# Kernel tuning notes

Measured on AMD Instinct MI355X. Metric: run time of the kernel, lower is better.

The kernel has to match this reference:

```python
import jax, jax.numpy as jnp
import numpy as np

B, T, I, H, O = 128, 1024, 256, 512, 256


def setup_inputs() -> dict:
    key = jax.random.key(0)
    ks = jax.random.split(key, 6)
    fan_gate = I + H  # kaiming-style scaling for stability over long scan
    return {
        "input_seq": jax.random.normal(ks[0], (B, T, I), dtype=jnp.float32),
        "W_f": jax.random.normal(ks[1], (H, fan_gate), dtype=jnp.float32) / np.sqrt(fan_gate),
        "b_f": jnp.zeros((H,), dtype=jnp.float32),
        "W_i": jax.random.normal(ks[2], (H, fan_gate), dtype=jnp.float32) / np.sqrt(fan_gate),
        "b_i": jnp.zeros((H,), dtype=jnp.float32),
        "W_C": jax.random.normal(ks[3], (H, fan_gate), dtype=jnp.float32) / np.sqrt(fan_gate),
        "b_C": jnp.zeros((H,), dtype=jnp.float32),
        "W_o": jax.random.normal(ks[4], (H, fan_gate), dtype=jnp.float32) / np.sqrt(fan_gate),
        "b_o": jnp.zeros((H,), dtype=jnp.float32),
        "W_lin": jax.random.normal(ks[5], (O, H), dtype=jnp.float32) / np.sqrt(H),
        "b_lin": jnp.zeros((O,), dtype=jnp.float32),
    }


def reference(input_seq, W_f, b_f, W_i, b_i, W_C, b_C, W_o, b_o, W_lin, b_lin):
    batch = input_seq.shape[0]
    hidden = W_f.shape[0]

    def step(carry, x_t):
        h, C = carry  # [B,H] each
        combined = jnp.concatenate([x_t, h], axis=1)  # [B, I+H]
        f_t = jax.nn.sigmoid(combined @ W_f.T + b_f)
        i_t = jax.nn.sigmoid(combined @ W_i.T + b_i)
        C_tilde = jnp.tanh(combined @ W_C.T + b_C)
        o_t = jax.nn.sigmoid(combined @ W_o.T + b_o)
        C_new = f_t * C + i_t * C_tilde
        h_new = o_t * jnp.tanh(C_new)
        return (h_new, C_new), None

    h0 = jnp.zeros((batch, hidden), dtype=input_seq.dtype)
    C0 = jnp.zeros((batch, hidden), dtype=input_seq.dtype)
    # scan over time: input_seq -> [T, B, I]
    (h_T, _), _ = jax.lax.scan(step, (h0, C0), jnp.swapaxes(input_seq, 0, 1))
    return h_T @ W_lin.T + b_lin  # [B, O]
```

## Files before the change

kernel.cpp:

```cpp
#include <hip/hip_runtime.h>

#define BB 128
#define TT 1024
#define II 256
#define HH 512
#define OO 256
#define KK 768

typedef _Float16 half8 __attribute__((ext_vector_type(8)));
typedef _Float16 half4v __attribute__((ext_vector_type(4)));
typedef float f32x4 __attribute__((ext_vector_type(4)));
typedef unsigned u32x4 __attribute__((ext_vector_type(4)));
typedef unsigned long long u64_t;

__device__ __forceinline__ float sigm(float x) { return 1.f / (1.f + __expf(-x)); }
__device__ __forceinline__ float tanhfast(float x) {
  float e = __expf(-2.f * fabsf(x));
  return copysignf((1.f - e) / (1.f + e), x);
}

__global__ void __launch_bounds__(64)
prep_w(const float* __restrict__ Wf, const float* __restrict__ Wi,
       const float* __restrict__ Wc, const float* __restrict__ Wo,
       _Float16* __restrict__ W16)
{
  const int bid = blockIdx.x;
  const int ks = bid % 24, tile = bid / 24;
  const int lane = threadIdx.x;
  const int r = lane & 15, q = lane >> 4;
  const int lu = r >> 2, g = r & 3;
  const int unit = tile * 4 + lu;
  const float* Wg = (g == 0) ? Wf : (g == 1) ? Wi : (g == 2) ? Wc : Wo;
  const float* src = Wg + (size_t)unit * KK + ks * 32 + q * 8;
  float4 w0 = *(const float4*)src;
  float4 w1 = *(const float4*)(src + 4);
  half8 h;
  h[0] = (_Float16)w0.x; h[1] = (_Float16)w0.y; h[2] = (_Float16)w0.z; h[3] = (_Float16)w0.w;
  h[4] = (_Float16)w1.x; h[5] = (_Float16)w1.y; h[6] = (_Float16)w1.z; h[7] = (_Float16)w1.w;
  *(half8*)(W16 + ((size_t)bid * 64 + lane) * 8) = h;
}

__global__ void __launch_bounds__(256)
prep_x(const float* __restrict__ x, _Float16* __restrict__ x16)
{
  const int t = blockIdx.x;
  for (int i = threadIdx.x; i < BB * II / 4; i += 256) {
    const int b = i >> 6, c4 = (i & 63) * 4;
    float4 v = *(const float4*)(x + ((size_t)b * TT + t) * II + c4);
    half4v h;
    h[0] = (_Float16)v.x; h[1] = (_Float16)v.y; h[2] = (_Float16)v.z; h[3] = (_Float16)v.w;
    *(half4v*)(x16 + ((size_t)t * BB + b) * II + c4) = h;
  }
}

__device__ __forceinline__ unsigned pack2(unsigned a, unsigned b) {
  return (a & 0xffffu) | (b << 16);
}
__device__ __forceinline__ unsigned badtag(u32x4 g, unsigned ex) {
  return ((g.x ^ ex) | (g.y ^ ex) | (g.z ^ ex) | (g.w ^ ex)) & 0xFFFF0000u;
}

__global__ void __launch_bounds__(256, 1)
lstm_persist(const _Float16* __restrict__ x16, const _Float16* __restrict__ W16,
             const float* __restrict__ bfp, const float* __restrict__ bip,
             const float* __restrict__ bcp, const float* __restrict__ bop,
             const float* __restrict__ Wlin, const float* __restrict__ blin,
             float* __restrict__ out,
             unsigned* __restrict__ hbuf)
{
  __shared__ __align__(16) char hsb[2][16 * 1024];

  const int gid = blockIdx.x;
  const int p = gid & 7;
  const int ugh = gid >> 3;
  const int tid = threadIdx.x;
  const int wn = tid >> 6, lane = tid & 63;
  const int r = lane & 15, q = lane >> 4;
  const int lu = r >> 2, g4 = r & 3;
  const int rsw = (r & 7) << 4;

  half8 wfrag[24];
  {
    const half8* wp = (const half8*)W16 + (size_t)(ugh * 4 + wn) * 24 * 64 + lane;
#pragma unroll
    for (int ks = 0; ks < 24; ++ks) wfrag[ks] = wp[ks * 64];
  }

  const int unit = ugh * 16 + wn * 4 + lu;
  const float bfv = bfp[unit], biv = bip[unit], bcv = bcp[unit], bov = bop[unit];
  float C = 0.0f;
  const int arow = p * 16 + r;

  int unit0[4];
#pragma unroll
  for (int j = 0; j < 4; ++j) unit0[j] = 8 * (lane ^ ((4 * j + wn) & 7));

  f32x4 accN = {0.f, 0.f, 0.f, 0.f};
  {
    const _Float16* xr = x16 + (size_t)arow * II + q * 8;
#pragma unroll
    for (int ks = 0; ks < 8; ++ks) {
      half8 a = *(const half8*)(xr + ks * 32);
      accN = __builtin_amdgcn_mfma_f32_16x16x32_f16(a, wfrag[ks], accN, 0, 0, 0);
    }
  }

  for (int t = 0; t < TT; ++t) {
    f32x4 acc = accN;
    const int buf = t & 1;

    if (t > 0) {
      const unsigned ex32 = (unsigned)t << 16;
      const unsigned* b0 = hbuf + ((size_t)(buf * BB + p * 16) + 0 + wn) * HH + unit0[0];
      const unsigned* b1 = hbuf + ((size_t)(buf * BB + p * 16) + 4 + wn) * HH + unit0[1];
      const unsigned* b2 = hbuf + ((size_t)(buf * BB + p * 16) + 8 + wn) * HH + unit0[2];
      const unsigned* b3 = hbuf + ((size_t)(buf * BB + p * 16) + 12 + wn) * HH + unit0[3];
      u32x4 G0, G1, G2, G3, G4, G5, G6, G7;
      for (int it = 0;; ++it) {
        if ((it & 1) == 0) {
          asm volatile(
            "global_load_dwordx4 %0, %8, off sc0\n\t"
            "global_load_dwordx4 %1, %8, off offset:16 sc0\n\t"
            "global_load_dwordx4 %2, %9, off sc0\n\t"
            "global_load_dwordx4 %3, %9, off offset:16 sc0\n\t"
            "global_load_dwordx4 %4, %10, off sc0\n\t"
            "global_load_dwordx4 %5, %10, off offset:16 sc0\n\t"
            "global_load_dwordx4 %6, %11, off sc0\n\t"
            "global_load_dwordx4 %7, %11, off offset:16 sc0\n\t"
            "s_waitcnt vmcnt(0)"
            : "=&v"(G0), "=&v"(G1), "=&v"(G2), "=&v"(G3),
              "=&v"(G4), "=&v"(G5), "=&v"(G6), "=&v"(G7)
            : "v"(b0), "v"(b1), "v"(b2), "v"(b3)
            : "memory");
        } else {
          const u64_t* pp;
          u64_t a0, a1, a2, a3;
#define LD4(bp, A, B)                                                            \
          pp = (const u64_t*)(bp);                                               \
          a0 = __hip_atomic_load(pp,     __ATOMIC_RELAXED, __HIP_MEMORY_SCOPE_AGENT); \
          a1 = __hip_atomic_load(pp + 1, __ATOMIC_RELAXED, __HIP_MEMORY_SCOPE_AGENT); \
          a2 = __hip_atomic_load(pp + 2, __ATOMIC_RELAXED, __HIP_MEMORY_SCOPE_AGENT); \
          a3 = __hip_atomic_load(pp + 3, __ATOMIC_RELAXED, __HIP_MEMORY_SCOPE_AGENT); \
          A = (u32x4){(unsigned)a0, (unsigned)(a0 >> 32), (unsigned)a1, (unsigned)(a1 >> 32)}; \
          B = (u32x4){(unsigned)a2, (unsigned)(a2 >> 32), (unsigned)a3, (unsigned)(a3 >> 32)};
          LD4(b0, G0, G1) LD4(b1, G2, G3) LD4(b2, G4, G5) LD4(b3, G6, G7)
#undef LD4
        }
        unsigned bad = badtag(G0, ex32) | badtag(G1, ex32) | badtag(G2, ex32) |
                       badtag(G3, ex32) | badtag(G4, ex32) | badtag(G5, ex32) |
                       badtag(G6, ex32) | badtag(G7, ex32);
        if (bad == 0) break;
        __builtin_amdgcn_s_sleep(1);
      }
      char* dst = hsb[buf] + tid * 16;
      *(u32x4*)(dst)          = (u32x4){pack2(G0.x, G0.y), pack2(G0.z, G0.w),
                                        pack2(G1.x, G1.y), pack2(G1.z, G1.w)};
      *(u32x4*)(dst + 4096)   = (u32x4){pack2(G2.x, G2.y), pack2(G2.z, G2.w),
                                        pack2(G3.x, G3.y), pack2(G3.z, G3.w)};
      *(u32x4*)(dst + 8192)   = (u32x4){pack2(G4.x, G4.y), pack2(G4.z, G4.w),
                                        pack2(G5.x, G5.y), pack2(G5.z, G5.w)};
      *(u32x4*)(dst + 12288)  = (u32x4){pack2(G6.x, G6.y), pack2(G6.z, G6.w),
                                        pack2(G7.x, G7.y), pack2(G7.z, G7.w)};
      __syncthreads();

      const char* hrow = hsb[buf] + r * 1024;
#pragma unroll
      for (int ks = 0; ks < 16; ++ks) {
        half8 a = *(const half8*)(hrow + ((ks * 64 + q * 16) ^ rsw));
        acc = __builtin_amdgcn_mfma_f32_16x16x32_f16(a, wfrag[8 + ks], acc, 0, 0, 0);
      }
    }

    float t1[4], sx[4], pg[4];
#pragma unroll
    for (int i = 0; i < 4; ++i) sx[i] = __shfl_xor(acc[i], 1);
#pragma unroll
    for (int i = 0; i < 4; ++i) t1[i] = ((i & 1) == (g4 & 1)) ? acc[i] : sx[i ^ 1];
#pragma unroll
    for (int i = 0; i < 4; ++i) sx[i] = __shfl_xor(t1[i], 2);
#pragma unroll
    for (int i = 0; i < 4; ++i) pg[i] = ((i & 2) == (g4 & 2)) ? t1[i] : sx[i ^ 2];

    C = sigm(pg[0] + bfv) * C + sigm(pg[1] + biv) * tanhfast(pg[2] + bcv);
    float hn = sigm(pg[3] + bov) * tanhfast(C);
    unsigned hv;
    { _Float16 a16 = (_Float16)hn; hv = (unsigned)__builtin_bit_cast(unsigned short, a16); }
    {
      unsigned val = ((unsigned)(t + 1) << 16) | hv;
      unsigned* sa = hbuf + ((size_t)(((t + 1) & 1)) * BB + p * 16 + q * 4 + g4) * HH + unit;
      asm volatile("global_store_dword %0, %1, off" :: "v"(sa), "v"(val) : "memory");
      __hip_atomic_store(sa, val, __ATOMIC_RELAXED, __HIP_MEMORY_SCOPE_AGENT);
    }

    if (t + 1 < TT) {
      accN = (f32x4){0.f, 0.f, 0.f, 0.f};
      const _Float16* xr = x16 + ((size_t)(t + 1) * BB + arow) * II + q * 8;
#pragma unroll
      for (int ks = 0; ks < 8; ++ks) {
        half8 a = *(const half8*)(xr + ks * 32);
        accN = __builtin_amdgcn_mfma_f32_16x16x32_f16(a, wfrag[ks], accN, 0, 0, 0);
      }
    }
  }

  {
    const int erow = p * 16 + (ugh >> 1);
    const int o0 = (ugh & 1) * 128;
    float* hf = (float*)hsb;
    const unsigned* hb = hbuf + (size_t)erow * HH;
#pragma unroll
    for (int k = 0; k < 2; ++k) {
      int u = tid + k * 256;
      unsigned v;
      for (;;) {
        v = __hip_atomic_load(hb + u, __ATOMIC_RELAXED, __HIP_MEMORY_SCOPE_AGENT);
        if ((v >> 16) == (unsigned)TT) break;
        __builtin_amdgcn_s_sleep(1);
      }
      hf[u] = (float)__builtin_bit_cast(_Float16, (unsigned short)(v & 0xffffu));
    }
    __syncthreads();
    if (tid < 128) {
      int o = o0 + tid;
      float a2 = blin[o];
      const float4* wr = (const float4*)(Wlin + (size_t)o * HH);
#pragma unroll 4
      for (int j = 0; j < 128; ++j) {
        float4 wv = wr[j];
        a2 += wv.x * hf[4 * j] + wv.y * hf[4 * j + 1] +
              wv.z * hf[4 * j + 2] + wv.w * hf[4 * j + 3];
      }
      out[(size_t)erow * OO + o] = a2;
    }
  }
}

extern "C" void kernel_launch(void* const* d_in, const int* in_sizes, int n_in,
                              void* d_out, int out_size, void* d_ws, size_t ws_size,
                              hipStream_t stream) {
  const float* x    = (const float*)d_in[0];
  const float* Wf   = (const float*)d_in[1];
  const float* bf_  = (const float*)d_in[2];
  const float* Wi   = (const float*)d_in[3];
  const float* bi_  = (const float*)d_in[4];
  const float* Wc   = (const float*)d_in[5];
  const float* bc_  = (const float*)d_in[6];
  const float* Wo   = (const float*)d_in[7];
  const float* bo_  = (const float*)d_in[8];
  const float* Wlin = (const float*)d_in[9];
  const float* blin = (const float*)d_in[10];
  float* out = (float*)d_out;

  unsigned*  hbuf = (unsigned*)((char*)d_ws + 65536);
  _Float16*  W16  = (_Float16*)((char*)d_ws + 1048576);
  _Float16*  x16  = (_Float16*)((char*)d_ws + 4194304);

  hipMemsetAsync((char*)d_ws + 65536, 0, 2u * BB * HH * 4u, stream);
  prep_w<<<dim3(128 * 24), dim3(64), 0, stream>>>(Wf, Wi, Wc, Wo, W16);
  prep_x<<<dim3(TT), dim3(256), 0, stream>>>(x, x16);

  void* args[] = {(void*)&x16, (void*)&W16, (void*)&bf_, (void*)&bi_, (void*)&bc_,
                  (void*)&bo_, (void*)&Wlin, (void*)&blin, (void*)&out, (void*)&hbuf};
  hipLaunchCooperativeKernel((const void*)lstm_persist, dim3(256), dim3(256),
                             args, 0, stream);
}
```

Before: 4.563 ms.

## Add per-wave readiness flags before polling tagged hidden state; split MFMA accumulator chain

Each wave now publishes a per-step counter flag after its h store (waiting on vmcnt first), and consumers poll 128 flags per batch group before loading the tagged hidden-state data. This replaces repeated wide polling of h buffers with cheap flag polling. The recurrent MFMA chain is also split into two independent accumulators to shorten the dependency chain. The extra store, the wait, and the flag round trip add latency to every timestep's critical path.

```diff
diff --git a/kernel.cpp b/kernel.cpp
--- a/kernel.cpp
+++ b/kernel.cpp
@@ -66,7 +66,8 @@
              const float* __restrict__ bcp, const float* __restrict__ bop,
              const float* __restrict__ Wlin, const float* __restrict__ blin,
              float* __restrict__ out,
-             unsigned* __restrict__ hbuf)
+             unsigned* __restrict__ hbuf,
+             unsigned* __restrict__ flags)
 {
   __shared__ __align__(16) char hsb[2][16 * 1024];
 
@@ -95,6 +96,10 @@
 #pragma unroll
   for (int j = 0; j < 4; ++j) unit0[j] = 8 * (lane ^ ((4 * j + wn) & 7));
 
+  const unsigned* fb0 = flags + p * 128 + lane;
+  const unsigned* fb1 = fb0 + 64;
+  unsigned* fa = flags + p * 128 + ugh * 4 + wn;
+
   f32x4 accN = {0.f, 0.f, 0.f, 0.f};
   {
     const _Float16* xr = x16 + (size_t)arow * II + q * 8;
@@ -110,6 +115,22 @@
     const int buf = t & 1;
 
     if (t > 0) {
+      for (int it = 0;; ++it) {
+        unsigned f0, f1;
+        if ((it & 1) == 0) {
+          asm volatile(
+            "global_load_dword %0, %2, off sc0\n\t"
+            "global_load_dword %1, %3, off sc0\n\t"
+            "s_waitcnt vmcnt(0)"
+            : "=&v"(f0), "=&v"(f1) : "v"(fb0), "v"(fb1) : "memory");
+        } else {
+          f0 = __hip_atomic_load(fb0, __ATOMIC_RELAXED, __HIP_MEMORY_SCOPE_AGENT);
+          f1 = __hip_atomic_load(fb1, __ATOMIC_RELAXED, __HIP_MEMORY_SCOPE_AGENT);
+        }
+        if (__all(f0 >= (unsigned)t && f1 >= (unsigned)t)) break;
+        __builtin_amdgcn_s_sleep(1);
+      }
+
       const unsigned ex32 = (unsigned)t << 16;
       const unsigned* b0 = hbuf + ((size_t)(buf * BB + p * 16) + 0 + wn) * HH + unit0[0];
       const unsigned* b1 = hbuf + ((size_t)(buf * BB + p * 16) + 4 + wn) * HH + unit0[1];
@@ -153,22 +174,27 @@
         __builtin_amdgcn_s_sleep(1);
       }
       char* dst = hsb[buf] + tid * 16;
-      *(u32x4*)(dst)          = (u32x4){pack2(G0.x, G0.y), pack2(G0.z, G0.w),
-                                        pack2(G1.x, G1.y), pack2(G1.z, G1.w)};
-      *(u32x4*)(dst + 4096)   = (u32x4){pack2(G2.x, G2.y), pack2(G2.z, G2.w),
-                                        pack2(G3.x, G3.y), pack2(G3.z, G3.w)};
-      *(u32x4*)(dst + 8192)   = (u32x4){pack2(G4.x, G4.y), pack2(G4.z, G4.w),
-                                        pack2(G5.x, G5.y), pack2(G5.z, G5.w)};
-      *(u32x4*)(dst + 12288)  = (u32x4){pack2(G6.x, G6.y), pack2(G6.z, G6.w),
-                                        pack2(G7.x, G7.y), pack2(G7.z, G7.w)};
+      *(u32x4*)(dst)         = (u32x4){pack2(G0.x, G0.y), pack2(G0.z, G0.w),
+                                       pack2(G1.x, G1.y), pack2(G1.z, G1.w)};
+      *(u32x4*)(dst + 4096)  = (u32x4){pack2(G2.x, G2.y), pack2(G2.z, G2.w),
+                                       pack2(G3.x, G3.y), pack2(G3.z, G3.w)};
+      *(u32x4*)(dst + 8192)  = (u32x4){pack2(G4.x, G4.y), pack2(G4.z, G4.w),
+                                       pack2(G5.x, G5.y), pack2(G5.z, G5.w)};
+      *(u32x4*)(dst + 12288) = (u32x4){pack2(G6.x, G6.y), pack2(G6.z, G6.w),
+                                       pack2(G7.x, G7.y), pack2(G7.z, G7.w)};
       __syncthreads();
 
       const char* hrow = hsb[buf] + r * 1024;
-#pragma unroll
-      for (int ks = 0; ks < 16; ++ks) {
-        half8 a = *(const half8*)(hrow + ((ks * 64 + q * 16) ^ rsw));
-        acc = __builtin_amdgcn_mfma_f32_16x16x32_f16(a, wfrag[8 + ks], acc, 0, 0, 0);
-      }
+      f32x4 acc2 = {0.f, 0.f, 0.f, 0.f};
+#pragma unroll
+      for (int ks = 0; ks < 16; ks += 2) {
+        half8 a0 = *(const half8*)(hrow + (((ks)     * 64 + q * 16) ^ rsw));
+        half8 a1 = *(const half8*)(hrow + (((ks + 1) * 64 + q * 16) ^ rsw));
+        acc  = __builtin_amdgcn_mfma_f32_16x16x32_f16(a0, wfrag[8 + ks], acc, 0, 0, 0);
+        acc2 = __builtin_amdgcn_mfma_f32_16x16x32_f16(a1, wfrag[9 + ks], acc2, 0, 0, 0);
+      }
+#pragma unroll
+      for (int i = 0; i < 4; ++i) acc[i] += acc2[i];
     }
 
     float t1[4], sx[4], pg[4];
@@ -190,6 +216,12 @@
       unsigned* sa = hbuf + ((size_t)(((t + 1) & 1)) * BB + p * 16 + q * 4 + g4) * HH + unit;
       asm volatile("global_store_dword %0, %1, off" :: "v"(sa), "v"(val) : "memory");
       __hip_atomic_store(sa, val, __ATOMIC_RELAXED, __HIP_MEMORY_SCOPE_AGENT);
+      asm volatile("s_waitcnt vmcnt(0)" ::: "memory");
+      if (lane == 0) {
+        unsigned fval = (unsigned)(t + 1);
+        asm volatile("global_store_dword %0, %1, off" :: "v"(fa), "v"(fval) : "memory");
+        __hip_atomic_store(fa, fval, __ATOMIC_RELAXED, __HIP_MEMORY_SCOPE_AGENT);
+      }
     }
 
     if (t + 1 < TT) {
@@ -251,16 +283,18 @@
   const float* blin = (const float*)d_in[10];
   float* out = (float*)d_out;
 
-  unsigned*  hbuf = (unsigned*)((char*)d_ws + 65536);
-  _Float16*  W16  = (_Float16*)((char*)d_ws + 1048576);
-  _Float16*  x16  = (_Float16*)((char*)d_ws + 4194304);
-
-  hipMemsetAsync((char*)d_ws + 65536, 0, 2u * BB * HH * 4u, stream);
+  unsigned*  flags = (unsigned*)((char*)d_ws + 32768);
+  unsigned*  hbuf  = (unsigned*)((char*)d_ws + 65536);
+  _Float16*  W16   = (_Float16*)((char*)d_ws + 1048576);
+  _Float16*  x16   = (_Float16*)((char*)d_ws + 4194304);
+
+  hipMemsetAsync((char*)d_ws + 32768, 0, 65536 - 32768 + 2u * BB * HH * 4u, stream);
   prep_w<<<dim3(128 * 24), dim3(64), 0, stream>>>(Wf, Wi, Wc, Wo, W16);
   prep_x<<<dim3(TT), dim3(256), 0, stream>>>(x, x16);
 
   void* args[] = {(void*)&x16, (void*)&W16, (void*)&bf_, (void*)&bi_, (void*)&bc_,
-                  (void*)&bo_, (void*)&Wlin, (void*)&blin, (void*)&out, (void*)&hbuf};
+                  (void*)&bo_, (void*)&Wlin, (void*)&blin, (void*)&out,
+                  (void*)&hbuf, (void*)&flags};
   hipLaunchCooperativeKernel((const void*)lstm_persist, dim3(256), dim3(256),
                              args, 0, stream);
 }
```

Result: slower. 8.223 ms (+80.2%).
